# Kernel optimization log

Measured on AMD Instinct MI355X. Metric: run time of the kernel, lower is better.

Reference implementation:

```python
import jax, jax.numpy as jnp
import numpy as np

N_NODES = 100000


def setup_inputs() -> dict:
    key = jax.random.key(0)
    k1, k2, k3 = jax.random.split(key, 3)
    embedding = jax.random.normal(k1, (N_NODES, 128), dtype=jnp.float32)
    # xavier-ish scale for 128-dim fan-in
    weights = jax.random.normal(k2, (2, 4, 128, 128), dtype=jnp.float32) * 0.088
    biases = jnp.zeros((2, 4, 128), dtype=jnp.float32)
    edges = jax.random.randint(k3, (4, 2, 150000), 0, N_NODES, dtype=jnp.int32)
    return {"embedding": embedding, "weights": weights, "biases": biases, "edges": edges}


def _hetero_conv(h, W, b, edges, n_nodes):
    """HeteroGraphConv(mean) over R relations; each GraphConv uses norm='both'.
    h: [N, d_in], W: [R, d_in, d_h], b: [R, d_h], edges: [R, 2, E]."""

    def per_rel(e, Wr, br):
        src, dst = e[0], e[1]
        ones = jnp.ones(src.shape, dtype=h.dtype)
        deg_out = jnp.maximum(jax.ops.segment_sum(ones, src, num_segments=n_nodes), 1.0)
        deg_in = jnp.maximum(jax.ops.segment_sum(ones, dst, num_segments=n_nodes), 1.0)
        # D_src^{-1/2} X W
        x = h * jax.lax.rsqrt(deg_out)[:, None]
        m = x @ Wr  # [N, d_h]
        # gather along edges, scatter-add to dst (A @ m)
        agg = jax.ops.segment_sum(m[src], dst, num_segments=n_nodes)
        return agg * jax.lax.rsqrt(deg_in)[:, None] + br

    outs = jax.vmap(per_rel)(edges, W, b)  # [R, N, d_h]
    return outs.mean(axis=0)


def reference(embedding, weights, biases, edges):
    n_nodes = embedding.shape[0]
    num_layers = weights.shape[0]
    h = embedding
    for i in range(num_layers):
        out = _hetero_conv(h, weights[i], biases[i], edges, n_nodes)
        out = jax.nn.leaky_relu(out, negative_slope=0.2)
        if i > 0:
            out = out + h  # residual (hidden == in, slice [:, :hidden] is identity)
        h = out
    return h
```

## Files before the change

### kernel.cpp

```cpp
#include <hip/hip_runtime.h>
#include <cstdint>
#include <cstddef>

#define N_NODES 100000
#define D 128
#define R 4
#define NE 150000
#define LAYERS 2
#define NROWS (R * N_NODES)
#define CAP 16
#define TILES (N_NODES / 16)
#define GRID 512
#define TPB 512

typedef __attribute__((ext_vector_type(8))) short bf16x8;
typedef __attribute__((ext_vector_type(4))) float f32x4;
typedef __attribute__((ext_vector_type(4))) int i32x4;
typedef __attribute__((ext_vector_type(4))) unsigned short u16x4;

__device__ __forceinline__ unsigned short f2bf(float x) {
  union { float f; unsigned int u; } v; v.f = x;
  unsigned int u = v.u;
  return (unsigned short)((u + 0x7fffu + ((u >> 16) & 1u)) >> 16);
}
__device__ __forceinline__ float bf2f(unsigned short u) {
  union { unsigned int i; float f; } v; v.i = ((unsigned int)u) << 16;
  return v.f;
}

__global__ void count_kernel(const int* __restrict__ edges, int* __restrict__ deg_i) {
  int e = blockIdx.x * blockDim.x + threadIdx.x;
  int r = blockIdx.y;
  if (e >= NE) return;
  int src = edges[(size_t)(r * 2) * NE + e];
  atomicAdd(&deg_i[r * N_NODES + src], 1);
}

__global__ void fill_kernel(const int* __restrict__ edges, const int* __restrict__ deg_i,
                            int* __restrict__ cursor, int2* __restrict__ rec) {
  int e = blockIdx.x * blockDim.x + threadIdx.x;
  int r = blockIdx.y;
  if (e >= NE) return;
  int src = edges[(size_t)(r * 2) * NE + e];
  int dst = edges[(size_t)(r * 2 + 1) * NE + e];
  float sc = rsqrtf(fmaxf((float)deg_i[r * N_NODES + src], 1.0f));
  int rowg = r * N_NODES + dst;
  int slot = atomicAdd(&cursor[rowg], 1);
  if (slot < CAP) rec[(size_t)rowg * CAP + slot] = make_int2(src, __float_as_int(sc));
}

__global__ void prep_kernel(const float* __restrict__ emb, const float* __restrict__ W,
                            const float* __restrict__ biases, const int* __restrict__ cursor,
                            unsigned short* __restrict__ hb, unsigned short* __restrict__ Wt,
                            float* __restrict__ bmean, float* __restrict__ s_in) {
  int t = blockIdx.x * blockDim.x + threadIdx.x;
  if (t < N_NODES * D / 4) {
    f32x4 v = *(const f32x4*)(emb + (size_t)t * 4);
    u16x4 o;
#pragma unroll
    for (int j = 0; j < 4; ++j) o[j] = f2bf(v[j]);
    *(u16x4*)(hb + (size_t)t * 4) = o;
  }
  if (t < LAYERS * R * D * D) {
    int k = t & 127;
    int c = (t >> 7) & 127;
    int lr = t >> 14;
    Wt[((size_t)lr << 14) | (c << 7) | k] = f2bf(W[((size_t)lr << 14) | (k << 7) | c]);
  }
  if (t < NROWS) s_in[t] = rsqrtf(fmaxf((float)cursor[t], 1.0f));
  if (t < LAYERS * D) {
    int l = t >> 7, cc = t & 127;
    float s = 0.f;
    for (int r = 0; r < R; ++r) s += biases[((size_t)l * R + r) * D + cc];
    bmean[t] = s * 0.25f;
  }
}

__global__ __launch_bounds__(TPB, 2) void fused_kernel(
    const unsigned short* __restrict__ hb,
    const int2* __restrict__ rec,
    const int* __restrict__ cnt,
    const float* __restrict__ s_in,
    const unsigned short* __restrict__ Wt,
    const float* __restrict__ bmean,
    const unsigned short* __restrict__ resid_bf,
    float* __restrict__ out_f,
    unsigned short* __restrict__ out_bf) {
  __shared__ unsigned short t_lds[2][R * 4 * 64 * 8];
  const int w = threadIdx.x >> 6;
  const int lane = threadIdx.x & 63;
  const int m = lane & 15;
  const int q = lane >> 4;
  const int bid = blockIdx.x;
  const int nt = (TILES - bid + GRID - 1) / GRID;

  if (w < 4) {
    const int r = w;
    for (int it = 0; it < nt + 1; ++it) {
      if (it < nt) {
        const int tile = bid + it * GRID;
        const int rowg = r * N_NODES + tile * 16 + m;
        const int2* rp = rec + (size_t)rowg * CAP;
        int n = cnt[rowg];
        n = (n > CAP) ? CAP : n;
        i32x4 r01 = *(const i32x4*)(rp);
        i32x4 r23 = *(const i32x4*)(rp + 2);
        int   srcs[4] = { r01.x, r01.z, r23.x, r23.z };
        float scs[4]  = { __int_as_float(r01.y), __int_as_float(r01.w),
                          __int_as_float(r23.y), __int_as_float(r23.w) };
#pragma unroll
        for (int e = 0; e < 4; ++e) {
          if (e >= n) { srcs[e] = 0; scs[e] = 0.f; }
        }
        float accf[4][8];
#pragma unroll
        for (int ks = 0; ks < 4; ++ks)
#pragma unroll
          for (int j = 0; j < 8; ++j) accf[ks][j] = 0.f;
#pragma unroll
        for (int e = 0; e < 4; ++e) {
          const unsigned short* hp = hb + (size_t)srcs[e] * D + q * 8;
#pragma unroll
          for (int ks = 0; ks < 4; ++ks) {
            bf16x8 a = *(const bf16x8*)(hp + ks * 32);
#pragma unroll
            for (int j = 0; j < 8; ++j)
              accf[ks][j] += scs[e] * bf2f((unsigned short)a[j]);
          }
        }
        for (int i = 4; i < n; i += 2) {
          i32x4 rr = *(const i32x4*)(rp + i);
          bool pairOk = (i + 1) < n;
          int  sA = rr.x;
          int  sB = pairOk ? rr.z : 0;
          float c0 = __int_as_float(rr.y);
          float c1 = pairOk ? __int_as_float(rr.w) : 0.f;
          const unsigned short* h0 = hb + (size_t)sA * D + q * 8;
          const unsigned short* h1 = hb + (size_t)sB * D + q * 8;
#pragma unroll
          for (int ks = 0; ks < 4; ++ks) {
            bf16x8 a0 = *(const bf16x8*)(h0 + ks * 32);
            bf16x8 a1 = *(const bf16x8*)(h1 + ks * 32);
#pragma unroll
            for (int j = 0; j < 8; ++j)
              accf[ks][j] += c0 * bf2f((unsigned short)a0[j]) + c1 * bf2f((unsigned short)a1[j]);
          }
        }
        unsigned short* dstp = &t_lds[it & 1][(((r * 4) << 6) + lane) * 8];
#pragma unroll
        for (int ks = 0; ks < 4; ++ks) {
          union { bf16x8 v; unsigned short s[8]; } u;
#pragma unroll
          for (int j = 0; j < 8; ++j) u.s[j] = f2bf(accf[ks][j]);
          *(bf16x8*)(dstp + (ks << 6) * 8) = u.v;
        }
      }
      __syncthreads();
    }
  } else {
    const int cw = w - 4;
    bf16x8 breg[R][4][2];
#pragma unroll
    for (int r = 0; r < R; ++r) {
      const unsigned short* wr = Wt + ((size_t)r << 14);
#pragma unroll
      for (int ks = 0; ks < 4; ++ks)
#pragma unroll
        for (int c = 0; c < 2; ++c) {
          int ct = cw * 2 + c;
          breg[r][ks][c] = *(const bf16x8*)(wr + ((ct * 16 + m) << 7) + ks * 32 + q * 8);
        }
    }
    for (int it = 0; it < nt + 1; ++it) {
      if (it > 0) {
        const int tile = bid + (it - 1) * GRID;
        const int pb = (it - 1) & 1;
        float oacc[2][4];
#pragma unroll
        for (int c = 0; c < 2; ++c)
#pragma unroll
          for (int i = 0; i < 4; ++i) oacc[c][i] = 0.f;
#pragma unroll
        for (int r = 0; r < R; ++r) {
          f32x4 acc2[2];
#pragma unroll
          for (int c = 0; c < 2; ++c) acc2[c] = (f32x4){0.f, 0.f, 0.f, 0.f};
#pragma unroll
          for (int ks = 0; ks < 4; ++ks) {
            bf16x8 a = *(const bf16x8*)&t_lds[pb][(((r * 4 + ks) << 6) + lane) * 8];
#pragma unroll
            for (int c = 0; c < 2; ++c)
              acc2[c] = __builtin_amdgcn_mfma_f32_16x16x32_bf16(a, breg[r][ks][c], acc2[c], 0, 0, 0);
          }
          f32x4 s = *(const f32x4*)(s_in + (size_t)r * N_NODES + tile * 16 + q * 4);
#pragma unroll
          for (int c = 0; c < 2; ++c)
#pragma unroll
            for (int i = 0; i < 4; ++i) oacc[c][i] += s[i] * acc2[c][i];
        }
#pragma unroll
        for (int c = 0; c < 2; ++c) {
          int colx = (cw * 2 + c) * 16 + m;
          float bm = bmean[colx];
#pragma unroll
          for (int i = 0; i < 4; ++i) {
            int row = tile * 16 + q * 4 + i;
            float v = oacc[c][i] * 0.25f + bm;
            v = (v >= 0.f) ? v : 0.2f * v;
            if (resid_bf) v += bf2f(resid_bf[(size_t)row * D + colx]);
            if (out_f) out_f[(size_t)row * D + colx] = v;
            else       out_bf[(size_t)row * D + colx] = f2bf(v);
          }
        }
      }
      __syncthreads();
    }
  }
}

extern "C" void kernel_launch(void* const* d_in, const int* in_sizes, int n_in,
                              void* d_out, int out_size, void* d_ws, size_t ws_size,
                              hipStream_t stream) {
  const float* emb    = (const float*)d_in[0];
  const float* W      = (const float*)d_in[1];
  const float* biases = (const float*)d_in[2];
  const int*   edges  = (const int*)d_in[3];
  float* out = (float*)d_out;
  char* ws = (char*)d_ws;

  size_t off = 0;
  auto alloc = [&](size_t bytes) { size_t o = off; off += (bytes + 255) & ~255ull; return o; };
  int* ints      = (int*)(ws + alloc((size_t)2 * NROWS * 4));
  int* deg_i     = ints;
  int* cursor    = ints + NROWS;
  size_t zero_bytes = off;
  int2* rec      = (int2*)(ws + alloc((size_t)NROWS * CAP * 8));
  float* s_in    = (float*)(ws + alloc((size_t)NROWS * 4));
  unsigned short* hb  = (unsigned short*)(ws + alloc((size_t)N_NODES * D * 2));
  unsigned short* hb2 = (unsigned short*)(ws + alloc((size_t)N_NODES * D * 2));
  unsigned short* Wt  = (unsigned short*)(ws + alloc((size_t)LAYERS * R * D * D * 2));
  float* bmean   = (float*)(ws + alloc((size_t)LAYERS * D * 4));
  (void)ws_size;

  hipMemsetAsync(ws, 0, zero_bytes, stream);
  count_kernel<<<dim3((NE + 255) / 256, R), 256, 0, stream>>>(edges, deg_i);
  fill_kernel<<<dim3((NE + 255) / 256, R), 256, 0, stream>>>(edges, deg_i, cursor, rec);
  prep_kernel<<<(N_NODES * D / 4 + 255) / 256, 256, 0, stream>>>(
      emb, W, biases, cursor, hb, Wt, bmean, s_in);

  fused_kernel<<<GRID, TPB, 0, stream>>>(
      hb, rec, cursor, s_in, Wt, bmean, nullptr, nullptr, hb2);
  fused_kernel<<<GRID, TPB, 0, stream>>>(
      hb2, rec, cursor, s_in, Wt + (size_t)R * D * D, bmean + D, hb2, out, nullptr);
}
```

Measured before the change: 346.6 us.

## Software-pipeline gather loads across tiles and split edge records into compact and overflow arrays

The gather warps now issue the bf16 row loads for the next tile before accumulating the current tile, using double-buffered registers so memory latency overlaps with compute. Edge records are split into a compact 4-slot-per-node array laid out by tile plus a separate overflow array, which shrinks the footprint of the common-case record reads. The grid is halved to 256 blocks so each block handles more tiles for the pipeline, and __syncthreads is replaced by an explicit lgkmcnt wait plus s_barrier. The extra live registers risk spills or lower occupancy, and the smaller grid may leave some compute units idle.

```diff
diff --git a/kernel.cpp b/kernel.cpp
--- a/kernel.cpp
+++ b/kernel.cpp
@@ -9,8 +9,9 @@
 #define LAYERS 2
 #define NROWS (R * N_NODES)
 #define CAP 16
+#define OVFS 12
 #define TILES (N_NODES / 16)
-#define GRID 512
+#define GRID 256
 #define TPB 512
 
 typedef __attribute__((ext_vector_type(8))) short bf16x8;
@@ -37,7 +38,8 @@
 }
 
 __global__ void fill_kernel(const int* __restrict__ edges, const int* __restrict__ deg_i,
-                            int* __restrict__ cursor, int2* __restrict__ rec) {
+                            int* __restrict__ cursor, int2* __restrict__ rec2,
+                            int2* __restrict__ ovf) {
   int e = blockIdx.x * blockDim.x + threadIdx.x;
   int r = blockIdx.y;
   if (e >= NE) return;
@@ -46,7 +48,12 @@
   float sc = rsqrtf(fmaxf((float)deg_i[r * N_NODES + src], 1.0f));
   int rowg = r * N_NODES + dst;
   int slot = atomicAdd(&cursor[rowg], 1);
-  if (slot < CAP) rec[(size_t)rowg * CAP + slot] = make_int2(src, __float_as_int(sc));
+  if (slot < 4) {
+    int tile = dst >> 4, mm = dst & 15;
+    rec2[(((size_t)(r * TILES + tile) * 16 + mm) << 2) + slot] = make_int2(src, __float_as_int(sc));
+  } else if (slot < CAP) {
+    ovf[(size_t)rowg * OVFS + (slot - 4)] = make_int2(src, __float_as_int(sc));
+  }
 }
 
 __global__ void prep_kernel(const float* __restrict__ emb, const float* __restrict__ W,
@@ -76,9 +83,108 @@
   }
 }
 
+__device__ __forceinline__ void p_loadrec(const int* __restrict__ cnt,
+                                          const int2* __restrict__ rec2,
+                                          int r, int t, int m,
+                                          int& cN, i32x4& r0, i32x4& r1) {
+  const int2* rp = rec2 + (((size_t)(r * TILES + t) * 16 + m) << 2);
+  cN = cnt[r * N_NODES + t * 16 + m];
+  r0 = *(const i32x4*)(rp);
+  r1 = *(const i32x4*)(rp + 2);
+}
+
+__device__ __forceinline__ int p_issue(const unsigned short* __restrict__ hb,
+                                       const int2* __restrict__ ovf,
+                                       int r, int t, int m, int q,
+                                       int cN, i32x4 r0, i32x4 r1,
+                                       float (&scs)[4], bf16x8 (&ld)[16], i32x4& tr) {
+  int n = cN > CAP ? CAP : cN;
+  int srcs[4] = { r0.x, r0.z, r1.x, r1.z };
+  float sc[4] = { __int_as_float(r0.y), __int_as_float(r0.w),
+                  __int_as_float(r1.y), __int_as_float(r1.w) };
+#pragma unroll
+  for (int e = 0; e < 4; ++e) {
+    if (e >= n) { srcs[e] = 0; sc[e] = 0.f; }
+    scs[e] = sc[e];
+  }
+#pragma unroll
+  for (int e = 0; e < 4; ++e) {
+    const unsigned short* hp = hb + (size_t)srcs[e] * D + q * 8;
+#pragma unroll
+    for (int ks = 0; ks < 4; ++ks) ld[e * 4 + ks] = *(const bf16x8*)(hp + ks * 32);
+  }
+  if (__builtin_expect(n > 4, 0))
+    tr = *(const i32x4*)(ovf + (size_t)(r * N_NODES + t * 16 + m) * OVFS);
+  return n;
+}
+
+__device__ __forceinline__ void p_accum(const unsigned short* __restrict__ hb,
+                                        const int2* __restrict__ ovf,
+                                        unsigned short* __restrict__ dstp,
+                                        int r, int t, int m, int q,
+                                        int n, const float (&scs)[4], const bf16x8 (&ld)[16],
+                                        i32x4 tr) {
+  float accf[4][8];
+#pragma unroll
+  for (int ks = 0; ks < 4; ++ks)
+#pragma unroll
+    for (int j = 0; j < 8; ++j) accf[ks][j] = 0.f;
+  if (__builtin_expect(n > 4, 0)) {
+    bool ok = n > 5;
+    int sA = tr.x;
+    int sB = ok ? tr.z : 0;
+    float c0 = __int_as_float(tr.y);
+    float c1 = ok ? __int_as_float(tr.w) : 0.f;
+    const unsigned short* h0 = hb + (size_t)sA * D + q * 8;
+    const unsigned short* h1 = hb + (size_t)sB * D + q * 8;
+#pragma unroll
+    for (int ks = 0; ks < 4; ++ks) {
+      bf16x8 a0 = *(const bf16x8*)(h0 + ks * 32);
+      bf16x8 a1 = *(const bf16x8*)(h1 + ks * 32);
+#pragma unroll
+      for (int j = 0; j < 8; ++j)
+        accf[ks][j] += c0 * bf2f((unsigned short)a0[j]) + c1 * bf2f((unsigned short)a1[j]);
+    }
+    const int2* op = ovf + (size_t)(r * N_NODES + t * 16 + m) * OVFS;
+    for (int i = 6; i < n; i += 2) {
+      i32x4 rr = *(const i32x4*)(op + (i - 4));
+      bool ok2 = (i + 1) < n;
+      int s0 = rr.x;
+      int s1 = ok2 ? rr.z : 0;
+      float d0 = __int_as_float(rr.y);
+      float d1 = ok2 ? __int_as_float(rr.w) : 0.f;
+      const unsigned short* g0 = hb + (size_t)s0 * D + q * 8;
+      const unsigned short* g1 = hb + (size_t)s1 * D + q * 8;
+#pragma unroll
+      for (int ks = 0; ks < 4; ++ks) {
+        bf16x8 a0 = *(const bf16x8*)(g0 + ks * 32);
+        bf16x8 a1 = *(const bf16x8*)(g1 + ks * 32);
+#pragma unroll
+        for (int j = 0; j < 8; ++j)
+          accf[ks][j] += d0 * bf2f((unsigned short)a0[j]) + d1 * bf2f((unsigned short)a1[j]);
+      }
+    }
+  }
+#pragma unroll
+  for (int e = 0; e < 4; ++e)
+#pragma unroll
+    for (int ks = 0; ks < 4; ++ks)
+#pragma unroll
+      for (int j = 0; j < 8; ++j)
+        accf[ks][j] += scs[e] * bf2f((unsigned short)ld[e * 4 + ks][j]);
+#pragma unroll
+  for (int ks = 0; ks < 4; ++ks) {
+    union { bf16x8 v; unsigned short s[8]; } u;
+#pragma unroll
+    for (int j = 0; j < 8; ++j) u.s[j] = f2bf(accf[ks][j]);
+    *(bf16x8*)(dstp + (ks << 6) * 8) = u.v;
+  }
+}
+
 __global__ __launch_bounds__(TPB, 2) void fused_kernel(
     const unsigned short* __restrict__ hb,
-    const int2* __restrict__ rec,
+    const int2* __restrict__ rec2,
+    const int2* __restrict__ ovf,
     const int* __restrict__ cnt,
     const float* __restrict__ s_in,
     const unsigned short* __restrict__ Wt,
@@ -96,67 +202,39 @@
 
   if (w < 4) {
     const int r = w;
-    for (int it = 0; it < nt + 1; ++it) {
-      if (it < nt) {
-        const int tile = bid + it * GRID;
-        const int rowg = r * N_NODES + tile * 16 + m;
-        const int2* rp = rec + (size_t)rowg * CAP;
-        int n = cnt[rowg];
-        n = (n > CAP) ? CAP : n;
-        i32x4 r01 = *(const i32x4*)(rp);
-        i32x4 r23 = *(const i32x4*)(rp + 2);
-        int   srcs[4] = { r01.x, r01.z, r23.x, r23.z };
-        float scs[4]  = { __int_as_float(r01.y), __int_as_float(r01.w),
-                          __int_as_float(r23.y), __int_as_float(r23.w) };
-#pragma unroll
-        for (int e = 0; e < 4; ++e) {
-          if (e >= n) { srcs[e] = 0; scs[e] = 0.f; }
-        }
-        float accf[4][8];
-#pragma unroll
-        for (int ks = 0; ks < 4; ++ks)
-#pragma unroll
-          for (int j = 0; j < 8; ++j) accf[ks][j] = 0.f;
-#pragma unroll
-        for (int e = 0; e < 4; ++e) {
-          const unsigned short* hp = hb + (size_t)srcs[e] * D + q * 8;
-#pragma unroll
-          for (int ks = 0; ks < 4; ++ks) {
-            bf16x8 a = *(const bf16x8*)(hp + ks * 32);
-#pragma unroll
-            for (int j = 0; j < 8; ++j)
-              accf[ks][j] += scs[e] * bf2f((unsigned short)a[j]);
-          }
-        }
-        for (int i = 4; i < n; i += 2) {
-          i32x4 rr = *(const i32x4*)(rp + i);
-          bool pairOk = (i + 1) < n;
-          int  sA = rr.x;
-          int  sB = pairOk ? rr.z : 0;
-          float c0 = __int_as_float(rr.y);
-          float c1 = pairOk ? __int_as_float(rr.w) : 0.f;
-          const unsigned short* h0 = hb + (size_t)sA * D + q * 8;
-          const unsigned short* h1 = hb + (size_t)sB * D + q * 8;
-#pragma unroll
-          for (int ks = 0; ks < 4; ++ks) {
-            bf16x8 a0 = *(const bf16x8*)(h0 + ks * 32);
-            bf16x8 a1 = *(const bf16x8*)(h1 + ks * 32);
-#pragma unroll
-            for (int j = 0; j < 8; ++j)
-              accf[ks][j] += c0 * bf2f((unsigned short)a0[j]) + c1 * bf2f((unsigned short)a1[j]);
-          }
-        }
-        unsigned short* dstp = &t_lds[it & 1][(((r * 4) << 6) + lane) * 8];
-#pragma unroll
-        for (int ks = 0; ks < 4; ++ks) {
-          union { bf16x8 v; unsigned short s[8]; } u;
-#pragma unroll
-          for (int j = 0; j < 8; ++j) u.s[j] = f2bf(accf[ks][j]);
-          *(bf16x8*)(dstp + (ks << 6) * 8) = u.v;
-        }
+    int cA, cB;
+    i32x4 rA0, rA1, rB0, rB1, trA, trB;
+    float scsA[4], scsB[4];
+    bf16x8 ldA[16], ldB[16];
+    int nA = 0, nB = 0;
+
+    p_loadrec(cnt, rec2, r, bid, m, cA, rA0, rA1);
+    nA = p_issue(hb, ovf, r, bid, m, q, cA, rA0, rA1, scsA, ldA, trA);
+    p_loadrec(cnt, rec2, r, bid + GRID, m, cB, rB0, rB1);
+
+    for (int it = 0; it < nt; ++it) {
+      const int tcur = bid + it * GRID;
+      unsigned short* dstp = &t_lds[it & 1][(((r * 4) << 6) + lane) * 8];
+      if ((it & 1) == 0) {
+        if (it + 1 < nt) {
+          nB = p_issue(hb, ovf, r, tcur + GRID, m, q, cB, rB0, rB1, scsB, ldB, trB);
+          int t2 = tcur + 2 * GRID; if (t2 >= TILES) t2 = bid;
+          p_loadrec(cnt, rec2, r, t2, m, cA, rA0, rA1);
+        }
+        p_accum(hb, ovf, dstp, r, tcur, m, q, nA, scsA, ldA, trA);
+      } else {
+        if (it + 1 < nt) {
+          nA = p_issue(hb, ovf, r, tcur + GRID, m, q, cA, rA0, rA1, scsA, ldA, trA);
+          int t2 = tcur + 2 * GRID; if (t2 >= TILES) t2 = bid;
+          p_loadrec(cnt, rec2, r, t2, m, cB, rB0, rB1);
+        }
+        p_accum(hb, ovf, dstp, r, tcur, m, q, nB, scsB, ldB, trB);
       }
-      __syncthreads();
-    }
+      asm volatile("s_waitcnt lgkmcnt(0)" ::: "memory");
+      __builtin_amdgcn_s_barrier();
+    }
+    asm volatile("s_waitcnt lgkmcnt(0)" ::: "memory");
+    __builtin_amdgcn_s_barrier();
   } else {
     const int cw = w - 4;
     bf16x8 breg[R][4][2];
@@ -213,7 +291,8 @@
           }
         }
       }
-      __syncthreads();
+      asm volatile("s_waitcnt lgkmcnt(0)" ::: "memory");
+      __builtin_amdgcn_s_barrier();
     }
   }
 }
@@ -234,7 +313,8 @@
   int* deg_i     = ints;
   int* cursor    = ints + NROWS;
   size_t zero_bytes = off;
-  int2* rec      = (int2*)(ws + alloc((size_t)NROWS * CAP * 8));
+  int2* rec2     = (int2*)(ws + alloc((size_t)R * TILES * 16 * 4 * 8));
+  int2* ovf      = (int2*)(ws + alloc((size_t)NROWS * OVFS * 8));
   float* s_in    = (float*)(ws + alloc((size_t)NROWS * 4));
   unsigned short* hb  = (unsigned short*)(ws + alloc((size_t)N_NODES * D * 2));
   unsigned short* hb2 = (unsigned short*)(ws + alloc((size_t)N_NODES * D * 2));
@@ -244,12 +324,12 @@
 
   hipMemsetAsync(ws, 0, zero_bytes, stream);
   count_kernel<<<dim3((NE + 255) / 256, R), 256, 0, stream>>>(edges, deg_i);
-  fill_kernel<<<dim3((NE + 255) / 256, R), 256, 0, stream>>>(edges, deg_i, cursor, rec);
+  fill_kernel<<<dim3((NE + 255) / 256, R), 256, 0, stream>>>(edges, deg_i, cursor, rec2, ovf);
   prep_kernel<<<(N_NODES * D / 4 + 255) / 256, 256, 0, stream>>>(
       emb, W, biases, cursor, hb, Wt, bmean, s_in);
 
   fused_kernel<<<GRID, TPB, 0, stream>>>(
-      hb, rec, cursor, s_in, Wt, bmean, nullptr, nullptr, hb2);
+      hb, rec2, ovf, cursor, s_in, Wt, bmean, nullptr, nullptr, hb2);
   fused_kernel<<<GRID, TPB, 0, stream>>>(
-      hb2, rec, cursor, s_in, Wt + (size_t)R * D * D, bmean + D, hb2, out, nullptr);
-}
+      hb2, rec2, ovf, cursor, s_in, Wt + (size_t)R * D * D, bmean + D, hb2, out, nullptr);
+}
```

Result: slower. 447.7 us (+29.2%).

## Split edge records into dense 4-slot array plus overflow, merge prep kernels

Applied to the files above, without the earlier changes.

Stores the first four incoming-edge records per destination row in a compact tile-ordered array and moves slots 4..15 to a separate overflow buffer, so the common-case gather reads a denser record region. Degree counting is merged into the embedding/weight prep kernel, and the separate s_in buffer is dropped in favour of recomputing rsqrt of the in-degree inside the fused kernel. This cuts one kernel launch and some memory traffic. The grid size is also halved. The price is a branchy overflow path and extra rsqrt work in the consumer warps.

```diff
diff --git a/kernel.cpp b/kernel.cpp
--- a/kernel.cpp
+++ b/kernel.cpp
@@ -9,8 +9,9 @@
 #define LAYERS 2
 #define NROWS (R * N_NODES)
 #define CAP 16
+#define OVFS 12
 #define TILES (N_NODES / 16)
-#define GRID 512
+#define GRID 256
 #define TPB 512
 
 typedef __attribute__((ext_vector_type(8))) short bf16x8;
@@ -28,16 +29,41 @@
   return v.f;
 }
 
-__global__ void count_kernel(const int* __restrict__ edges, int* __restrict__ deg_i) {
-  int e = blockIdx.x * blockDim.x + threadIdx.x;
-  int r = blockIdx.y;
-  if (e >= NE) return;
-  int src = edges[(size_t)(r * 2) * NE + e];
-  atomicAdd(&deg_i[r * N_NODES + src], 1);
+__global__ void prep1_kernel(const float* __restrict__ emb, const float* __restrict__ W,
+                             const float* __restrict__ biases, const int* __restrict__ edges,
+                             int* __restrict__ deg_i, unsigned short* __restrict__ hb,
+                             unsigned short* __restrict__ Wt, float* __restrict__ bmean) {
+  int t = blockIdx.x * blockDim.x + threadIdx.x;
+  if (t < N_NODES * D / 4) {
+    f32x4 v = *(const f32x4*)(emb + (size_t)t * 4);
+    u16x4 o;
+#pragma unroll
+    for (int j = 0; j < 4; ++j) o[j] = f2bf(v[j]);
+    *(u16x4*)(hb + (size_t)t * 4) = o;
+  }
+  if (t < NE * R) {
+    int r = t / NE;
+    int e = t - r * NE;
+    int src = edges[(size_t)(r * 2) * NE + e];
+    atomicAdd(&deg_i[r * N_NODES + src], 1);
+  }
+  if (t < LAYERS * R * D * D) {
+    int k = t & 127;
+    int c = (t >> 7) & 127;
+    int lr = t >> 14;
+    Wt[((size_t)lr << 14) | (c << 7) | k] = f2bf(W[((size_t)lr << 14) | (k << 7) | c]);
+  }
+  if (t < LAYERS * D) {
+    int l = t >> 7, cc = t & 127;
+    float s = 0.f;
+    for (int r = 0; r < R; ++r) s += biases[((size_t)l * R + r) * D + cc];
+    bmean[t] = s * 0.25f;
+  }
 }
 
 __global__ void fill_kernel(const int* __restrict__ edges, const int* __restrict__ deg_i,
-                            int* __restrict__ cursor, int2* __restrict__ rec) {
+                            int* __restrict__ cursor, int2* __restrict__ rec2,
+                            int2* __restrict__ ovf) {
   int e = blockIdx.x * blockDim.x + threadIdx.x;
   int r = blockIdx.y;
   if (e >= NE) return;
@@ -46,41 +72,19 @@
   float sc = rsqrtf(fmaxf((float)deg_i[r * N_NODES + src], 1.0f));
   int rowg = r * N_NODES + dst;
   int slot = atomicAdd(&cursor[rowg], 1);
-  if (slot < CAP) rec[(size_t)rowg * CAP + slot] = make_int2(src, __float_as_int(sc));
-}
-
-__global__ void prep_kernel(const float* __restrict__ emb, const float* __restrict__ W,
-                            const float* __restrict__ biases, const int* __restrict__ cursor,
-                            unsigned short* __restrict__ hb, unsigned short* __restrict__ Wt,
-                            float* __restrict__ bmean, float* __restrict__ s_in) {
-  int t = blockIdx.x * blockDim.x + threadIdx.x;
-  if (t < N_NODES * D / 4) {
-    f32x4 v = *(const f32x4*)(emb + (size_t)t * 4);
-    u16x4 o;
-#pragma unroll
-    for (int j = 0; j < 4; ++j) o[j] = f2bf(v[j]);
-    *(u16x4*)(hb + (size_t)t * 4) = o;
-  }
-  if (t < LAYERS * R * D * D) {
-    int k = t & 127;
-    int c = (t >> 7) & 127;
-    int lr = t >> 14;
-    Wt[((size_t)lr << 14) | (c << 7) | k] = f2bf(W[((size_t)lr << 14) | (k << 7) | c]);
-  }
-  if (t < NROWS) s_in[t] = rsqrtf(fmaxf((float)cursor[t], 1.0f));
-  if (t < LAYERS * D) {
-    int l = t >> 7, cc = t & 127;
-    float s = 0.f;
-    for (int r = 0; r < R; ++r) s += biases[((size_t)l * R + r) * D + cc];
-    bmean[t] = s * 0.25f;
+  if (slot < 4) {
+    rec2[(((size_t)(r * TILES + (dst >> 4)) * 16 + (dst & 15)) << 2) + slot] =
+        make_int2(src, __float_as_int(sc));
+  } else if (slot < CAP) {
+    ovf[(size_t)rowg * OVFS + (slot - 4)] = make_int2(src, __float_as_int(sc));
   }
 }
 
 __global__ __launch_bounds__(TPB, 2) void fused_kernel(
     const unsigned short* __restrict__ hb,
-    const int2* __restrict__ rec,
+    const int2* __restrict__ rec2,
+    const int2* __restrict__ ovf,
     const int* __restrict__ cnt,
-    const float* __restrict__ s_in,
     const unsigned short* __restrict__ Wt,
     const float* __restrict__ bmean,
     const unsigned short* __restrict__ resid_bf,
@@ -100,7 +104,7 @@
       if (it < nt) {
         const int tile = bid + it * GRID;
         const int rowg = r * N_NODES + tile * 16 + m;
-        const int2* rp = rec + (size_t)rowg * CAP;
+        const int2* rp = rec2 + (((size_t)(r * TILES + tile) * 16 + m) << 2);
         int n = cnt[rowg];
         n = (n > CAP) ? CAP : n;
         i32x4 r01 = *(const i32x4*)(rp);
@@ -128,22 +132,25 @@
               accf[ks][j] += scs[e] * bf2f((unsigned short)a[j]);
           }
         }
-        for (int i = 4; i < n; i += 2) {
-          i32x4 rr = *(const i32x4*)(rp + i);
-          bool pairOk = (i + 1) < n;
-          int  sA = rr.x;
-          int  sB = pairOk ? rr.z : 0;
-          float c0 = __int_as_float(rr.y);
-          float c1 = pairOk ? __int_as_float(rr.w) : 0.f;
-          const unsigned short* h0 = hb + (size_t)sA * D + q * 8;
-          const unsigned short* h1 = hb + (size_t)sB * D + q * 8;
-#pragma unroll
-          for (int ks = 0; ks < 4; ++ks) {
-            bf16x8 a0 = *(const bf16x8*)(h0 + ks * 32);
-            bf16x8 a1 = *(const bf16x8*)(h1 + ks * 32);
-#pragma unroll
-            for (int j = 0; j < 8; ++j)
-              accf[ks][j] += c0 * bf2f((unsigned short)a0[j]) + c1 * bf2f((unsigned short)a1[j]);
+        if (__builtin_expect(n > 4, 0)) {
+          const int2* op = ovf + (size_t)rowg * OVFS;
+          for (int i = 4; i < n; i += 2) {
+            i32x4 rr = *(const i32x4*)(op + (i - 4));
+            bool pairOk = (i + 1) < n;
+            int  sA = rr.x;
+            int  sB = pairOk ? rr.z : 0;
+            float c0 = __int_as_float(rr.y);
+            float c1 = pairOk ? __int_as_float(rr.w) : 0.f;
+            const unsigned short* h0 = hb + (size_t)sA * D + q * 8;
+            const unsigned short* h1 = hb + (size_t)sB * D + q * 8;
+#pragma unroll
+            for (int ks = 0; ks < 4; ++ks) {
+              bf16x8 a0 = *(const bf16x8*)(h0 + ks * 32);
+              bf16x8 a1 = *(const bf16x8*)(h1 + ks * 32);
+#pragma unroll
+              for (int j = 0; j < 8; ++j)
+                accf[ks][j] += c0 * bf2f((unsigned short)a0[j]) + c1 * bf2f((unsigned short)a1[j]);
+            }
           }
         }
         unsigned short* dstp = &t_lds[it & 1][(((r * 4) << 6) + lane) * 8];
@@ -192,11 +199,12 @@
             for (int c = 0; c < 2; ++c)
               acc2[c] = __builtin_amdgcn_mfma_f32_16x16x32_bf16(a, breg[r][ks][c], acc2[c], 0, 0, 0);
           }
-          f32x4 s = *(const f32x4*)(s_in + (size_t)r * N_NODES + tile * 16 + q * 4);
+          i32x4 ci = *(const i32x4*)(cnt + (size_t)r * N_NODES + tile * 16 + q * 4);
 #pragma unroll
           for (int c = 0; c < 2; ++c)
 #pragma unroll
-            for (int i = 0; i < 4; ++i) oacc[c][i] += s[i] * acc2[c][i];
+            for (int i = 0; i < 4; ++i)
+              oacc[c][i] += rsqrtf(fmaxf((float)ci[i], 1.0f)) * acc2[c][i];
         }
 #pragma unroll
         for (int c = 0; c < 2; ++c) {
@@ -234,8 +242,8 @@
   int* deg_i     = ints;
   int* cursor    = ints + NROWS;
   size_t zero_bytes = off;
-  int2* rec      = (int2*)(ws + alloc((size_t)NROWS * CAP * 8));
-  float* s_in    = (float*)(ws + alloc((size_t)NROWS * 4));
+  int2* rec2     = (int2*)(ws + alloc((size_t)R * TILES * 16 * 4 * 8));
+  int2* ovf      = (int2*)(ws + alloc((size_t)NROWS * OVFS * 8));
   unsigned short* hb  = (unsigned short*)(ws + alloc((size_t)N_NODES * D * 2));
   unsigned short* hb2 = (unsigned short*)(ws + alloc((size_t)N_NODES * D * 2));
   unsigned short* Wt  = (unsigned short*)(ws + alloc((size_t)LAYERS * R * D * D * 2));
@@ -243,13 +251,12 @@
   (void)ws_size;
 
   hipMemsetAsync(ws, 0, zero_bytes, stream);
-  count_kernel<<<dim3((NE + 255) / 256, R), 256, 0, stream>>>(edges, deg_i);
-  fill_kernel<<<dim3((NE + 255) / 256, R), 256, 0, stream>>>(edges, deg_i, cursor, rec);
-  prep_kernel<<<(N_NODES * D / 4 + 255) / 256, 256, 0, stream>>>(
-      emb, W, biases, cursor, hb, Wt, bmean, s_in);
+  prep1_kernel<<<(N_NODES * D / 4 + 255) / 256, 256, 0, stream>>>(
+      emb, W, biases, edges, deg_i, hb, Wt, bmean);
+  fill_kernel<<<dim3((NE + 255) / 256, R), 256, 0, stream>>>(edges, deg_i, cursor, rec2, ovf);
 
   fused_kernel<<<GRID, TPB, 0, stream>>>(
-      hb, rec, cursor, s_in, Wt, bmean, nullptr, nullptr, hb2);
+      hb, rec2, ovf, cursor, Wt, bmean, nullptr, nullptr, hb2);
   fused_kernel<<<GRID, TPB, 0, stream>>>(
-      hb2, rec, cursor, s_in, Wt + (size_t)R * D * D, bmean + D, hb2, out, nullptr);
-}
+      hb2, rec2, ovf, cursor, Wt + (size_t)R * D * D, bmean + D, hb2, out, nullptr);
+}
```

Result: no change. 340.1 us (-1.9%).
